# Kernel optimization log

Measured on AMD Instinct MI355X. Metric: run time of the kernel, lower is better.

The kernel has to match this reference:

```python
import jax, jax.numpy as jnp
import numpy as np

B, T, D, H, F, Q = 256, 512, 64, 1024, 8, 3

def setup_inputs() -> dict:
    key = jax.random.key(0)
    ks = jax.random.split(key, 6)
    scale = 0.05
    x  = jax.random.normal(ks[0], (B, T, D), dtype=jnp.float32)
    Wx = jax.random.normal(ks[1], (D, 4 * H), dtype=jnp.float32) * scale  # input->gates (no bias, flax dense_i)
    Wh = jax.random.normal(ks[2], (H, 4 * H), dtype=jnp.float32) * scale  # hidden->gates
    b  = jnp.zeros((4 * H,), dtype=jnp.float32)                           # bias on hidden path (flax dense_h)
    Wr = jax.random.normal(ks[3], (F, H, Q), dtype=jnp.float32) * scale   # per-feature Dense(H -> 1*Q)
    br = jnp.zeros((F, Q), dtype=jnp.float32)
    return {"x": x, "Wx": Wx, "Wh": Wh, "b": b, "Wr": Wr, "br": br}

def _lstm_last_hidden(x, Wx, Wh, b):
    # x: (B, T, D) -> scan over time, return final hidden (B, H)
    Bn = x.shape[0]
    h0 = jnp.zeros((Bn, H), dtype=x.dtype)
    c0 = jnp.zeros((Bn, H), dtype=x.dtype)
    # precompute input projection for all timesteps: (T, B, 4H)
    xz = jnp.einsum('btd,dk->tbk', x, Wx)
    def step(carry, xz_t):
        h, c = carry
        z = xz_t + h @ Wh + b                      # (B, 4H)
        i, f, g, o = jnp.split(z, 4, axis=-1)      # flax gate order: i, f, g, o
        i = jax.nn.sigmoid(i)
        f = jax.nn.sigmoid(f)
        g = jnp.tanh(g)
        o = jax.nn.sigmoid(o)
        c_new = f * c + i * g
        h_new = o * jnp.tanh(c_new)
        return (h_new, c_new), None
    (h_fin, c_fin), _ = jax.lax.scan(step, (h0, c0), xz)
    return h_fin

def reference(x, Wx, Wh, b, Wr, br):
    h_last = _lstm_last_hidden(x, Wx, Wh, b)            # (B, H)
    # per-feature small Dense heads, stacked: (B, F, Q)
    out = jnp.einsum('bh,fhq->bfq', h_last, Wr) + br
    return out.astype(jnp.float32)
```

## Files before the change

### kernel.cpp

```cpp
#include <hip/hip_runtime.h>
#include <hip/hip_bf16.h>

#define B_   256
#define T_   512
#define D_   64
#define H_   1024
#define NG   4096
#define KTOT 1088
#define WPAD 1096

typedef __attribute__((ext_vector_type(8)))  short short8;
typedef __attribute__((ext_vector_type(4)))  float f32x4;
typedef __attribute__((ext_vector_type(16))) float f32x16;

static __device__ __forceinline__ float tanh_clamped(float u) {
  u = fminf(fmaxf(u, -15.0f), 15.0f);
  float e = __expf(-2.0f * u);
  return (1.0f - e) / (1.0f + e);
}
static __device__ __forceinline__ unsigned short f2bf(float f) {
  union { float f; unsigned int u; } v; v.f = f;
  unsigned int r = (v.u + 0x7FFFu + ((v.u >> 16) & 1u)) >> 16;
  return (unsigned short)r;
}

__global__ void k_zero_flags(int* flags) {
  int gid = blockIdx.x * 256 + threadIdx.x;
  if (gid < 4096) flags[gid] = 0;
}

__global__ void k_pack_w(const float* __restrict__ Wx, const float* __restrict__ Wh,
                         unsigned short* __restrict__ Wp) {
  __shared__ float tile[64][65];
  int nt = blockIdx.x & 63;
  int kt = blockIdx.x >> 6;
  int tx = threadIdx.x & 63, ty = threadIdx.x >> 6;
#pragma unroll
  for (int i = 0; i < 16; ++i) {
    int kl = i * 4 + ty;
    int k  = kt * 64 + kl;
    int n  = nt * 64 + tx;
    int oc = ((n & 3) << 10) | (n >> 2);
    float v = (k < D_) ? Wx[k * NG + oc] : Wh[(k - D_) * NG + oc];
    tile[kl][tx] = v;
  }
  __syncthreads();
#pragma unroll
  for (int i = 0; i < 16; ++i) {
    int nl = i * 4 + ty;
    int kl = tx;
    Wp[(size_t)(nt * 64 + nl) * KTOT + kt * 64 + kl] = f2bf(tile[kl][nl]);
  }
}

__global__ void k_pack_x(const float* __restrict__ x, unsigned short* __restrict__ xbt) {
  int gid = blockIdx.x * 256 + threadIdx.x;
  int b  = gid & 255;
  int kk = (gid >> 8) & 7;
  int t  = gid >> 11;
  const float* src = x + ((size_t)b * T_ + t) * 64 + kk * 8;
  short8 v;
#pragma unroll
  for (int i = 0; i < 8; ++i) v[i] = (short)f2bf(src[i]);
  *(short8*)(xbt + (size_t)gid * 8) = v;
}

__launch_bounds__(256, 1)
__global__ void k_scan(const unsigned short* __restrict__ Wp,
                       const unsigned short* __restrict__ xbt,
                       unsigned short* __restrict__ hbt,
                       float* __restrict__ hf,
                       const float* __restrict__ bias,
                       int* __restrict__ flags) {
  __shared__ unsigned short Wl[64 * WPAD];
  __shared__ float exch[4][16][64];
  __shared__ unsigned short hstage[4][32][8];
  __shared__ int blkcnt;
  const int tid  = threadIdx.x;
  const int bid  = blockIdx.x;
  const int m    = (bid >> 1) & 3;
  const int nt   = ((bid >> 3) << 1) | (bid & 1);
  const int n0   = nt * 64;
  const int wave = tid >> 6;
  const int lane = tid & 63;
  const int wr = wave >> 1, wc = wave & 1;

  if (tid == 0) blkcnt = 0;
  for (int i = tid; i < 64 * (KTOT / 8); i += 256) {
    int c  = i / (KTOT / 8);
    int kk = i - c * (KTOT / 8);
    short8 v = *(const short8*)(Wp + (size_t)(n0 + c) * KTOT + kk * 8);
    *(short8*)((char*)Wl + c * (WPAD * 2) + kk * 16) = v;
  }
  __syncthreads();

  const int khalf = lane >> 5;
  const int rowA  = m * 64 + wr * 32 + (lane & 31);
  const int colB  = wc * 32 + (lane & 31);
  const int n     = n0 + colB;
  const int oc    = ((n & 3) << 10) | (n >> 2);
  const float bv  = bias[oc];
  const int s     = lane & 3;
  const int q     = (lane & 31) >> 2;
  const int jH    = n >> 2;
  const char* WlK = (const char*)Wl + (size_t)(wc * 32 + (lane & 31)) * (WPAD * 2) + khalf * 16;
  const char* WlS = (const char*)Wl + (size_t)((1 - wc) * 32 + (lane & 31)) * (WPAD * 2) + khalf * 16;

  float c_state[16];
#pragma unroll
  for (int r = 0; r < 16; ++r) c_state[r] = 0.0f;

  int* myflag = flags + (m * 64 + nt) * 16;
  const int pidx = (lane < 32) ? (wc * 32 + lane) : nt;
  int* pollp  = flags + (m * 64 + pidx) * 16;

  const unsigned int voff0 = (unsigned)(khalf * 4096 + rowA * 16);
  const unsigned int vstore0 = (unsigned)(((nt * 2 + wc) * 256 + m * 64 + wr * 32) * 16);

  for (int t = 0; t < T_; ++t) {
    f32x16 accK;
#pragma unroll
    for (int r = 0; r < 16; ++r) accK[r] = bv;

#pragma unroll
    for (int kt = 0; kt < 4; ++kt) {
      int kkx = t * 8 + kt * 2 + khalf;
      short8 a  = *(const short8*)(xbt + (size_t)kkx * 2048 + rowA * 8);
      short8 b8 = *(const short8*)(WlK + kt * 32);
      accK = __builtin_amdgcn_mfma_f32_32x32x16_bf16(a, b8, accK, 0, 0, 0);
    }

    if (t > 0) {
      __builtin_amdgcn_sched_barrier(0);
      for (;;) {
        int v = __hip_atomic_load(pollp, __ATOMIC_RELAXED, __HIP_MEMORY_SCOPE_AGENT);
        if (__all(v >= t)) break;
      }
      const unsigned short* hsrc = hbt + (size_t)((t + 1) & 1) * 128 * 2048;

      short8 aH[32];
#pragma unroll
      for (int j = 0; j < 32; ++j) {
        unsigned int vo = voff0 + (unsigned)((wc * 32 + j) * 8192);
        asm volatile("global_load_dwordx4 %0, %1, %2 sc0 sc1"
                     : "=v"(aH[j]) : "v"(vo), "s"(hsrc));
      }
      f32x16 accS;
#pragma unroll
      for (int r = 0; r < 16; ++r) accS[r] = 0.0f;

#pragma unroll
      for (int g = 0; g < 4; ++g) {
        switch (g) {
          case 0: asm volatile("s_waitcnt vmcnt(24)" ::: "memory"); break;
          case 1: asm volatile("s_waitcnt vmcnt(16)" ::: "memory"); break;
          case 2: asm volatile("s_waitcnt vmcnt(8)"  ::: "memory"); break;
          case 3: asm volatile("s_waitcnt vmcnt(0)"  ::: "memory"); break;
        }
        __builtin_amdgcn_sched_barrier(0);
#pragma unroll
        for (int jj = 0; jj < 8; ++jj) {
          int j  = g * 8 + jj;
          int kt = wc * 32 + j;
          short8 bk = *(const short8*)(WlK + 128 + kt * 32);
          short8 bs = *(const short8*)(WlS + 128 + kt * 32);
          accK = __builtin_amdgcn_mfma_f32_32x32x16_bf16(aH[j], bk, accK, 0, 0, 0);
          accS = __builtin_amdgcn_mfma_f32_32x32x16_bf16(aH[j], bs, accS, 0, 0, 0);
        }
      }

#pragma unroll
      for (int r = 0; r < 16; ++r) exch[wave][r][lane] = accS[r];
      __syncthreads();
#pragma unroll
      for (int r = 0; r < 16; ++r) accK[r] += exch[wave ^ 1][r][lane];
      __syncthreads();
    }

#pragma unroll
    for (int r = 0; r < 16; ++r) {
      float z  = accK[r];
      float u  = (s == 2) ? z : 0.5f * z;
      float tv = tanh_clamped(u);
      float av = (s == 2) ? tv : 0.5f * (1.0f + tv);
      float x1 = __shfl_xor(av, 1);
      float x2 = __shfl_xor(av, 2);
      float x3 = __shfl_xor(av, 3);
      float i_ = (s == 0) ? av : (s == 1) ? x1 : (s == 2) ? x2 : x3;
      float f_ = (s == 1) ? av : (s == 0) ? x1 : (s == 3) ? x2 : x3;
      float g_ = (s == 2) ? av : (s == 3) ? x1 : (s == 0) ? x2 : x3;
      float o_ = (s == 3) ? av : (s == 2) ? x1 : (s == 1) ? x2 : x3;
      float cn = f_ * c_state[r] + i_ * g_;
      c_state[r] = cn;
      float hn = o_ * tanh_clamped(cn);
      if (s == 0) {
        int rloc = 4 * khalf + (r & 3) + 8 * (r >> 2);
        if (t < T_ - 1) {
          hstage[wave][rloc][q] = f2bf(hn);
        } else {
          hf[(size_t)(m * 64 + wr * 32 + rloc) * H_ + jH] = hn;
        }
      }
    }

    if (t < T_ - 1) {
      asm volatile("s_waitcnt lgkmcnt(0)" ::: "memory");
      unsigned short* hdst = hbt + (size_t)(t & 1) * 128 * 2048;
      if (lane < 32) {
        f32x4 v = *(const f32x4*)&hstage[wave][lane][0];
        unsigned int vo = vstore0 + (unsigned)(lane * 16);
        asm volatile("global_store_dwordx4 %0, %1, %2 sc0 sc1"
                     :: "v"(vo), "v"(v), "s"(hdst) : "memory");
      }
      asm volatile("s_waitcnt vmcnt(0)" ::: "memory");
      if (lane == 0) {
        int old = __hip_atomic_fetch_add(&blkcnt, 1, __ATOMIC_RELAXED,
                                         __HIP_MEMORY_SCOPE_WORKGROUP);
        if (old == 4 * t + 3) {
          __hip_atomic_store(myflag, t + 1, __ATOMIC_RELAXED, __HIP_MEMORY_SCOPE_AGENT);
        }
      }
    }
  }
}

__global__ void k_head(const float* __restrict__ hf, const float* __restrict__ Wr,
                       const float* __restrict__ br, float* __restrict__ out) {
  int bf = blockIdx.x;
  int b = bf >> 3, f = bf & 7;
  int lane = threadIdx.x;
  float s0 = 0.f, s1 = 0.f, s2 = 0.f;
  for (int j = lane; j < H_; j += 64) {
    float h = hf[(size_t)b * H_ + j];
    const float* w = Wr + ((size_t)f * H_ + j) * 3;
    s0 = fmaf(h, w[0], s0); s1 = fmaf(h, w[1], s1); s2 = fmaf(h, w[2], s2);
  }
#pragma unroll
  for (int o = 32; o >= 1; o >>= 1) {
    s0 += __shfl_xor(s0, o); s1 += __shfl_xor(s1, o); s2 += __shfl_xor(s2, o);
  }
  if (lane == 0) {
    out[bf * 3 + 0] = s0 + br[f * 3 + 0];
    out[bf * 3 + 1] = s1 + br[f * 3 + 1];
    out[bf * 3 + 2] = s2 + br[f * 3 + 2];
  }
}

extern "C" void kernel_launch(void* const* d_in, const int* in_sizes, int n_in,
                              void* d_out, int out_size, void* d_ws, size_t ws_size,
                              hipStream_t stream) {
  const float* x    = (const float*)d_in[0];
  const float* Wx   = (const float*)d_in[1];
  const float* Wh   = (const float*)d_in[2];
  const float* bias = (const float*)d_in[3];
  const float* Wr   = (const float*)d_in[4];
  const float* br   = (const float*)d_in[5];
  float* out = (float*)d_out;

  char* ws = (char*)d_ws;
  unsigned short* Wp  = (unsigned short*)ws;
  unsigned short* xbt = (unsigned short*)(ws + 8912896);
  unsigned short* hbt = (unsigned short*)(ws + 8912896 + 16777216);
  float* hf           = (float*)(ws + 8912896 + 16777216 + 1048576);
  int* flags          = (int*)(ws + 8912896 + 16777216 + 1048576 + 1048576);

  k_zero_flags<<<16, 256, 0, stream>>>(flags);
  k_pack_w<<<17 * 64, 256, 0, stream>>>(Wx, Wh, Wp);
  k_pack_x<<<4096, 256, 0, stream>>>(x, xbt);
  k_scan<<<256, 256, 0, stream>>>(Wp, xbt, hbt, hf, bias, flags);
  k_head<<<2048, 64, 0, stream>>>(hf, Wr, br, out);
}
```

Before: 3.917 ms.

## Prefetch next-step x tiles during flag publish, use DPP quad permutes

The input-projection A operands for the next timestep are loaded into registers right after the h store, before the flag handshake. This overlaps their latency with the cross-block synchronisation, and the publish wait changes to vmcnt(4) so the prefetch is left in flight. The gate-gathering __shfl_xor calls become DPP quad permutes, which avoids LDS-based shuffles. The flag store becomes an inline global_store with sc0 sc1. The change adds register pressure and relies on the vmcnt counting being correct for the store to be visible before the flag.

New measurement: 3.664 ms. -6.5%, faster.

```diff
diff --git a/kernel.cpp b/kernel.cpp
--- a/kernel.cpp
+++ b/kernel.cpp
@@ -22,6 +22,14 @@
   union { float f; unsigned int u; } v; v.f = f;
   unsigned int r = (v.u + 0x7FFFu + ((v.u >> 16) & 1u)) >> 16;
   return (unsigned short)r;
+}
+
+template <int CTRL>
+static __device__ __forceinline__ float qperm(float v) {
+  union { float f; int i; } a, b;
+  a.f = v;
+  b.i = __builtin_amdgcn_update_dpp(0, a.i, CTRL, 0xF, 0xF, true);
+  return b.f;
 }
 
 __global__ void k_zero_flags(int* flags) {
@@ -117,17 +125,30 @@
   const unsigned int voff0 = (unsigned)(khalf * 4096 + rowA * 16);
   const unsigned int vstore0 = (unsigned)(((nt * 2 + wc) * 256 + m * 64 + wr * 32) * 16);
 
+  unsigned int vx[4];
+#pragma unroll
+  for (int f = 0; f < 4; ++f) vx[f] = (unsigned)((f * 2 + khalf) * 4096 + rowA * 16);
+
+  short8 ax[4];
+  {
+    const unsigned short* xb = xbt;
+#pragma unroll
+    for (int f = 0; f < 4; ++f)
+      asm volatile("global_load_dwordx4 %0, %1, %2"
+                   : "=v"(ax[f]) : "v"(vx[f]), "s"(xb));
+  }
+
   for (int t = 0; t < T_; ++t) {
     f32x16 accK;
 #pragma unroll
     for (int r = 0; r < 16; ++r) accK[r] = bv;
 
+    asm volatile("s_waitcnt vmcnt(0)" ::: "memory");
+    __builtin_amdgcn_sched_barrier(0);
 #pragma unroll
     for (int kt = 0; kt < 4; ++kt) {
-      int kkx = t * 8 + kt * 2 + khalf;
-      short8 a  = *(const short8*)(xbt + (size_t)kkx * 2048 + rowA * 8);
       short8 b8 = *(const short8*)(WlK + kt * 32);
-      accK = __builtin_amdgcn_mfma_f32_32x32x16_bf16(a, b8, accK, 0, 0, 0);
+      accK = __builtin_amdgcn_mfma_f32_32x32x16_bf16(ax[kt], b8, accK, 0, 0, 0);
     }
 
     if (t > 0) {
@@ -183,9 +204,9 @@
       float u  = (s == 2) ? z : 0.5f * z;
       float tv = tanh_clamped(u);
       float av = (s == 2) ? tv : 0.5f * (1.0f + tv);
-      float x1 = __shfl_xor(av, 1);
-      float x2 = __shfl_xor(av, 2);
-      float x3 = __shfl_xor(av, 3);
+      float x1 = qperm<0xB1>(av);
+      float x2 = qperm<0x4E>(av);
+      float x3 = qperm<0x1B>(av);
       float i_ = (s == 0) ? av : (s == 1) ? x1 : (s == 2) ? x2 : x3;
       float f_ = (s == 1) ? av : (s == 0) ? x1 : (s == 3) ? x2 : x3;
       float g_ = (s == 2) ? av : (s == 3) ? x1 : (s == 0) ? x2 : x3;
@@ -212,12 +233,21 @@
         asm volatile("global_store_dwordx4 %0, %1, %2 sc0 sc1"
                      :: "v"(vo), "v"(v), "s"(hdst) : "memory");
       }
-      asm volatile("s_waitcnt vmcnt(0)" ::: "memory");
+      {
+        const unsigned short* xb = xbt + (size_t)(t + 1) * 16384;
+#pragma unroll
+        for (int f = 0; f < 4; ++f)
+          asm volatile("global_load_dwordx4 %0, %1, %2"
+                       : "=v"(ax[f]) : "v"(vx[f]), "s"(xb));
+      }
+      asm volatile("s_waitcnt vmcnt(4)" ::: "memory");
       if (lane == 0) {
         int old = __hip_atomic_fetch_add(&blkcnt, 1, __ATOMIC_RELAXED,
                                          __HIP_MEMORY_SCOPE_WORKGROUP);
         if (old == 4 * t + 3) {
-          __hip_atomic_store(myflag, t + 1, __ATOMIC_RELAXED, __HIP_MEMORY_SCOPE_AGENT);
+          unsigned int fv = (unsigned)(t + 1);
+          asm volatile("global_store_dword %0, %1, %2 sc0 sc1"
+                       :: "v"(0u), "v"(fv), "s"(myflag) : "memory");
         }
       }
     }
```
